# Performance work log

Hardware: AMD Instinct MI355X
Metric: run time of the kernel (lower is better)

Reference implementation:

```python
import jax, jax.numpy as jnp
import numpy as np

B, S, D_MODEL, D_INNER = 64, 128, 1024, 1024


def setup_inputs() -> dict:
    key = jax.random.key(0)
    ks = jax.random.split(key, 10)
    sc = 0.02
    return {
        "embeddings": jax.random.normal(ks[0], (B, S, D_MODEL), dtype=jnp.float32),
        "Wq": jax.random.normal(ks[1], (D_MODEL, D_INNER), dtype=jnp.float32) * sc,
        "bq": jnp.zeros((D_INNER,), dtype=jnp.float32),
        "Wk": jax.random.normal(ks[2], (D_MODEL, D_INNER), dtype=jnp.float32) * sc,
        "bk": jnp.zeros((D_INNER,), dtype=jnp.float32),
        "Wv": jax.random.normal(ks[3], (D_MODEL, D_INNER), dtype=jnp.float32) * sc,
        "bv": jnp.zeros((D_INNER,), dtype=jnp.float32),
        "w": jax.random.normal(ks[4], (S, S), dtype=jnp.float32) * sc,
        "Wo": jax.random.normal(ks[5], (D_INNER, D_MODEL), dtype=jnp.float32) * sc,
        "bo": jnp.zeros((D_MODEL,), dtype=jnp.float32),
    }


def reference(embeddings, Wq, bq, Wk, bk, Wv, bv, w, Wo, bo):
    # embeddings: [B, S, Dm]
    seq_len = embeddings.shape[1]
    q = embeddings @ Wq + bq          # [B, S, Di]
    k = embeddings @ Wk + bk
    v = embeddings @ Wv + bv

    max_k = jnp.max(k, axis=1, keepdims=True)   # [B, 1, Di]
    exp_k = jnp.exp(k - max_k)                  # [B, S, Di]

    max_w = jnp.max(w, axis=1, keepdims=True)   # [S, 1]
    wn = w - max_w                              # [S, S]
    tril = jnp.tril(jnp.ones((seq_len, seq_len), dtype=bool))
    wn = jnp.where(tril, wn[:seq_len, :seq_len], -jnp.inf)
    # torch.einsum('bjj,bjd->bjd', exp_w, x) picks the DIAGONAL of exp_w
    # (repeated subscript j) and multiplies elementwise along the seq dim.
    diag_w = jnp.exp(jnp.diagonal(wn))          # [S]; tril diagonal is True so finite
    dw = diag_w[None, :, None]                  # [1, S, 1]

    numerator = dw * (exp_k * v)                # [B, S, Di]
    denominator = dw * exp_k                    # [B, S, Di]
    out = jax.nn.sigmoid(q) * (numerator / denominator)
    return out @ Wo + bo                        # [B, S, Dm]
```

## Files before the change

### kernel.cpp

```cpp
#include <hip/hip_runtime.h>


typedef short bf16x8 __attribute__((ext_vector_type(8)));
typedef float f32x4  __attribute__((ext_vector_type(4)));

__device__ __forceinline__ short f2bf(float f) {
  union { float f; unsigned u; } x; x.f = f;
  unsigned r = x.u + 0x7fffu + ((x.u >> 16) & 1u);
  return (short)(r >> 16);
}

struct alignas(16) S8 { short v[8]; };

#define GLDS(g, l) \
  __builtin_amdgcn_global_load_lds((const __attribute__((address_space(1))) void*)(g), \
                                   (__attribute__((address_space(3))) void*)(l), 16, 0, 0)

__global__ __launch_bounds__(256) void prep_kernel(
    const float* __restrict__ emb, const float* __restrict__ Wq, const float* __restrict__ Wv,
    const float* __restrict__ Wo, short* __restrict__ embB, short* __restrict__ WqvT,
    short* __restrict__ WoT) {
  __shared__ float tr[32 * 33];
  const int t = threadIdx.x;
  const int bid = blockIdx.x;
  const int gdim = gridDim.x;

  for (size_t i = (size_t)bid * 256 + t; i < 1048576; i += (size_t)gdim * 256) {
    const float4* p = (const float4*)emb + i * 2;
    float4 a = p[0], b = p[1];
    S8 s;
    s.v[0] = f2bf(a.x); s.v[1] = f2bf(a.y); s.v[2] = f2bf(a.z); s.v[3] = f2bf(a.w);
    s.v[4] = f2bf(b.x); s.v[5] = f2bf(b.y); s.v[6] = f2bf(b.z); s.v[7] = f2bf(b.w);
    ((S8*)embB)[i] = s;
  }

  int tx = t & 31, ty = t >> 5;
  for (int z = bid; z < 3072; z += gdim) {
    const float* in = (z < 1024) ? Wq : (z < 2048) ? Wv : Wo;
    short* op = (z < 1024) ? WqvT : (z < 2048) ? (WqvT + 1048576) : WoT;
    int ti = z & 1023;
    int bx = (ti & 31) * 32, by = (ti >> 5) * 32;
    __syncthreads();
#pragma unroll
    for (int i = 0; i < 32; i += 8)
      tr[(ty + i) * 33 + tx] = in[(size_t)(by + ty + i) * 1024 + bx + tx];
    __syncthreads();
#pragma unroll
    for (int i = 0; i < 32; i += 8)
      op[(size_t)(bx + ty + i) * 1024 + by + tx] = f2bf(tr[tx * 33 + ty + i]);
  }
}

__global__ __launch_bounds__(256) void gemm_qv_kernel(
    const short* __restrict__ A, const short* __restrict__ BT,
    const float* __restrict__ bq, const float* __restrict__ bv, short* __restrict__ X) {
  __shared__ short As[128 * 64];
  __shared__ short Bqs[64 * 64];
  __shared__ short Bvs[64 * 64];
  const int t = threadIdx.x;
  const int lane = t & 63;
  const int w = t >> 6;
  const int l16 = lane & 15;
  const int quad = lane >> 4;
  const int bm = blockIdx.x * 128;
  const int bn = blockIdx.y * 64;
  const int wm = (w & 1) * 64;
  const int wn = (w >> 1) * 32;

  const int r8 = t >> 3;
  const int swe = ((t & 7) ^ (r8 & 7)) * 8;
  const short* pA0 = A + (size_t)(bm + r8) * 1024 + swe;
  const short* pA1 = pA0 + 32 * 1024;
  const short* pA2 = pA0 + 64 * 1024;
  const short* pA3 = pA0 + 96 * 1024;
  const short* pBq0 = BT + (size_t)(bn + r8) * 1024 + swe;
  const short* pBq1 = pBq0 + 32 * 1024;
  const short* pBv0 = BT + (size_t)(1024 + bn + r8) * 1024 + swe;
  const short* pBv1 = pBv0 + 32 * 1024;
  short* lA = As + w * 512;
  short* lBq = Bqs + w * 512;
  short* lBv = Bvs + w * 512;

  const int qsw0 = (quad ^ (l16 & 7)) * 8;
  const int qsw1 = ((quad + 4) ^ (l16 & 7)) * 8;
  const short* fA0 = As + (wm + l16) * 64 + qsw0;
  const short* fA1 = As + (wm + l16) * 64 + qsw1;
  const short* fq0 = Bqs + (wn + l16) * 64 + qsw0;
  const short* fq1 = Bqs + (wn + l16) * 64 + qsw1;
  const short* fv0 = Bvs + (wn + l16) * 64 + qsw0;
  const short* fv1 = Bvs + (wn + l16) * 64 + qsw1;

  f32x4 accq[4][2] = {};
  f32x4 accv[4][2] = {};

  for (int it = 0; it < 16; ++it) {
    GLDS(pA0, lA); GLDS(pA1, lA + 2048); GLDS(pA2, lA + 4096); GLDS(pA3, lA + 6144);
    GLDS(pBq0, lBq); GLDS(pBq1, lBq + 2048);
    GLDS(pBv0, lBv); GLDS(pBv1, lBv + 2048);
    pA0 += 64; pA1 += 64; pA2 += 64; pA3 += 64;
    pBq0 += 64; pBq1 += 64; pBv0 += 64; pBv1 += 64;
    __syncthreads();

#pragma unroll
    for (int h = 0; h < 2; h++) {
      const short* fA = h ? fA1 : fA0;
      const short* fq = h ? fq1 : fq0;
      const short* fv = h ? fv1 : fv0;
      bf16x8 av[4], bqf[2], bvf[2];
#pragma unroll
      for (int i = 0; i < 4; i++) av[i] = *(const bf16x8*)(fA + i * 1024);
#pragma unroll
      for (int j = 0; j < 2; j++) {
        bqf[j] = *(const bf16x8*)(fq + j * 1024);
        bvf[j] = *(const bf16x8*)(fv + j * 1024);
      }
#pragma unroll
      for (int i = 0; i < 4; i++)
#pragma unroll
        for (int j = 0; j < 2; j++) {
          accq[i][j] = __builtin_amdgcn_mfma_f32_16x16x32_bf16(av[i], bqf[j], accq[i][j], 0, 0, 0);
          accv[i][j] = __builtin_amdgcn_mfma_f32_16x16x32_bf16(av[i], bvf[j], accv[i][j], 0, 0, 0);
        }
    }
    __syncthreads();
  }

#pragma unroll
  for (int j = 0; j < 2; j++) {
    int col = bn + wn + j * 16 + l16;
    float bql = bq[col], bvl = bv[col];
#pragma unroll
    for (int i = 0; i < 4; i++)
#pragma unroll
      for (int r = 0; r < 4; r++) {
        int row = bm + wm + i * 16 + quad * 4 + r;
        float q = accq[i][j][r] + bql;
        float v = accv[i][j][r] + bvl;
        float s = 1.0f / (1.0f + __expf(-q));
        X[(size_t)row * 1024 + col] = f2bf(s * v);
      }
  }
}

__global__ __launch_bounds__(256) void gemm_bt_kernel(
    const short* __restrict__ A, const short* __restrict__ BT, float* __restrict__ C,
    const float* __restrict__ bias) {
  __shared__ short As[128 * 64];
  __shared__ short Bs[128 * 64];
  const int t = threadIdx.x;
  const int lane = t & 63;
  const int w = t >> 6;
  const int l16 = lane & 15;
  const int quad = lane >> 4;
  const int bm = blockIdx.x * 128;
  const int bn = blockIdx.y * 128;
  const int wm = (w & 1) * 64;
  const int wn = (w >> 1) * 64;

  const int r8 = t >> 3;
  const int swe = ((t & 7) ^ (r8 & 7)) * 8;
  const short* pA0 = A + (size_t)(bm + r8) * 1024 + swe;
  const short* pA1 = pA0 + 32 * 1024;
  const short* pA2 = pA0 + 64 * 1024;
  const short* pA3 = pA0 + 96 * 1024;
  const short* pB0 = BT + (size_t)(bn + r8) * 1024 + swe;
  const short* pB1 = pB0 + 32 * 1024;
  const short* pB2 = pB0 + 64 * 1024;
  const short* pB3 = pB0 + 96 * 1024;
  short* lA = As + w * 512;
  short* lB = Bs + w * 512;

  const int qsw0 = (quad ^ (l16 & 7)) * 8;
  const int qsw1 = ((quad + 4) ^ (l16 & 7)) * 8;
  const short* fA0 = As + (wm + l16) * 64 + qsw0;
  const short* fA1 = As + (wm + l16) * 64 + qsw1;
  const short* fB0 = Bs + (wn + l16) * 64 + qsw0;
  const short* fB1 = Bs + (wn + l16) * 64 + qsw1;

  f32x4 acc[4][4] = {};

  for (int it = 0; it < 16; ++it) {
    GLDS(pA0, lA); GLDS(pA1, lA + 2048); GLDS(pA2, lA + 4096); GLDS(pA3, lA + 6144);
    GLDS(pB0, lB); GLDS(pB1, lB + 2048); GLDS(pB2, lB + 4096); GLDS(pB3, lB + 6144);
    pA0 += 64; pA1 += 64; pA2 += 64; pA3 += 64;
    pB0 += 64; pB1 += 64; pB2 += 64; pB3 += 64;
    __syncthreads();

#pragma unroll
    for (int h = 0; h < 2; h++) {
      const short* fA = h ? fA1 : fA0;
      const short* fB = h ? fB1 : fB0;
      bf16x8 av[4], bw[4];
#pragma unroll
      for (int i = 0; i < 4; i++) av[i] = *(const bf16x8*)(fA + i * 1024);
#pragma unroll
      for (int j = 0; j < 4; j++) bw[j] = *(const bf16x8*)(fB + j * 1024);
#pragma unroll
      for (int i = 0; i < 4; i++)
#pragma unroll
        for (int j = 0; j < 4; j++)
          acc[i][j] = __builtin_amdgcn_mfma_f32_16x16x32_bf16(av[i], bw[j], acc[i][j], 0, 0, 0);
    }
    __syncthreads();
  }

#pragma unroll
  for (int j = 0; j < 4; j++) {
    int col = bn + wn + j * 16 + l16;
    float bl = bias[col];
#pragma unroll
    for (int i = 0; i < 4; i++)
#pragma unroll
      for (int r = 0; r < 4; r++) {
        int row = bm + wm + i * 16 + quad * 4 + r;
        C[(size_t)row * 1024 + col] = acc[i][j][r] + bl;
      }
  }
}

extern "C" void kernel_launch(void* const* d_in, const int* in_sizes, int n_in,
                              void* d_out, int out_size, void* d_ws, size_t ws_size,
                              hipStream_t stream) {
  const float* emb = (const float*)d_in[0];
  const float* Wq  = (const float*)d_in[1];
  const float* bq  = (const float*)d_in[2];
  const float* Wv  = (const float*)d_in[5];
  const float* bv  = (const float*)d_in[6];
  const float* Wo  = (const float*)d_in[8];
  const float* bo  = (const float*)d_in[9];
  float* out = (float*)d_out;

  char* ws = (char*)d_ws;
  short* embB = (short*)(ws);
  short* X    = (short*)(ws + 16777216);
  short* WqvT = (short*)(ws + 33554432);
  short* WoT  = (short*)(ws + 37748736);

  prep_kernel<<<1024, 256, 0, stream>>>(emb, Wq, Wv, Wo, embB, WqvT, WoT);
  gemm_qv_kernel<<<dim3(64, 16), 256, 0, stream>>>(embB, WqvT, bq, bv, X);
  gemm_bt_kernel<<<dim3(64, 8), 256, 0, stream>>>(X, WoT, out, bo);
}
```

Before: 168.9 us.

## Fuse fp32-to-bf16 embedding conversion into QV GEMM A-tile loading

Drops the separate pass that converts the 32MB fp32 embedding tensor to bf16. The QV GEMM now loads fp32 A tiles through registers, packs them to bf16 with a perm-based rounding, and stores them into LDS itself, which removes one full write and re-read of the activations. The prep kernel now only transposes weights, one tile per block. In exchange, A is loaded synchronously through registers instead of direct global-to-LDS, and each of the 16 N-blocks re-reads fp32 A, doubling A traffic per GEMM. The new rounding also drops round-to-nearest-even tie handling.

```diff
diff --git a/kernel.cpp b/kernel.cpp
--- a/kernel.cpp
+++ b/kernel.cpp
@@ -10,49 +10,48 @@
   return (short)(r >> 16);
 }
 
+__device__ __forceinline__ unsigned pkbf(float f0, float f1) {
+  unsigned a = __float_as_uint(f1) + 0x8000u;
+  unsigned b = __float_as_uint(f0) + 0x8000u;
+  return __builtin_amdgcn_perm(a, b, 0x07060302u);
+}
+
 struct alignas(16) S8 { short v[8]; };
+
+__device__ __forceinline__ S8 pack8(float4 x, float4 y) {
+  union { unsigned d[4]; S8 s; } u;
+  u.d[0] = pkbf(x.x, x.y); u.d[1] = pkbf(x.z, x.w);
+  u.d[2] = pkbf(y.x, y.y); u.d[3] = pkbf(y.z, y.w);
+  return u.s;
+}
 
 #define GLDS(g, l) \
   __builtin_amdgcn_global_load_lds((const __attribute__((address_space(1))) void*)(g), \
                                    (__attribute__((address_space(3))) void*)(l), 16, 0, 0)
 
 __global__ __launch_bounds__(256) void prep_kernel(
-    const float* __restrict__ emb, const float* __restrict__ Wq, const float* __restrict__ Wv,
-    const float* __restrict__ Wo, short* __restrict__ embB, short* __restrict__ WqvT,
-    short* __restrict__ WoT) {
+    const float* __restrict__ Wq, const float* __restrict__ Wv, const float* __restrict__ Wo,
+    short* __restrict__ WqvT, short* __restrict__ WoT) {
   __shared__ float tr[32 * 33];
   const int t = threadIdx.x;
-  const int bid = blockIdx.x;
-  const int gdim = gridDim.x;
-
-  for (size_t i = (size_t)bid * 256 + t; i < 1048576; i += (size_t)gdim * 256) {
-    const float4* p = (const float4*)emb + i * 2;
-    float4 a = p[0], b = p[1];
-    S8 s;
-    s.v[0] = f2bf(a.x); s.v[1] = f2bf(a.y); s.v[2] = f2bf(a.z); s.v[3] = f2bf(a.w);
-    s.v[4] = f2bf(b.x); s.v[5] = f2bf(b.y); s.v[6] = f2bf(b.z); s.v[7] = f2bf(b.w);
-    ((S8*)embB)[i] = s;
-  }
-
-  int tx = t & 31, ty = t >> 5;
-  for (int z = bid; z < 3072; z += gdim) {
-    const float* in = (z < 1024) ? Wq : (z < 2048) ? Wv : Wo;
-    short* op = (z < 1024) ? WqvT : (z < 2048) ? (WqvT + 1048576) : WoT;
-    int ti = z & 1023;
-    int bx = (ti & 31) * 32, by = (ti >> 5) * 32;
-    __syncthreads();
-#pragma unroll
-    for (int i = 0; i < 32; i += 8)
-      tr[(ty + i) * 33 + tx] = in[(size_t)(by + ty + i) * 1024 + bx + tx];
-    __syncthreads();
-#pragma unroll
-    for (int i = 0; i < 32; i += 8)
-      op[(size_t)(bx + ty + i) * 1024 + by + tx] = f2bf(tr[tx * 33 + ty + i]);
-  }
+  const int z = blockIdx.x;
+  const float* in = (z < 1024) ? Wq : (z < 2048) ? Wv : Wo;
+  short* op = (z < 1024) ? WqvT : (z < 2048) ? (WqvT + 1048576) : WoT;
+  const int ti = z & 1023;
+  const int bx = (ti & 31) * 32, by = (ti >> 5) * 32;
+  const int tx = t & 31, ty = t >> 5;
+#pragma unroll
+  for (int i = 0; i < 32; i += 8)
+    tr[(ty + i) * 33 + tx] = in[(size_t)(by + ty + i) * 1024 + bx + tx];
+  __syncthreads();
+#pragma unroll
+  for (int i = 0; i < 32; i += 8)
+    op[(size_t)(bx + ty + i) * 1024 + by + tx] = f2bf(tr[tx * 33 + ty + i]);
 }
 
 __global__ __launch_bounds__(256) void gemm_qv_kernel(
-    const short* __restrict__ A, const short* __restrict__ BT,
+    const float* __restrict__ A,
+    const short* __restrict__ BT,
     const float* __restrict__ bq, const float* __restrict__ bv, short* __restrict__ X) {
   __shared__ short As[128 * 64];
   __shared__ short Bqs[64 * 64];
@@ -68,16 +67,18 @@
   const int wn = (w >> 1) * 32;
 
   const int r8 = t >> 3;
+  const int ch = (t & 7) ^ (r8 & 7);
+  const float* gA0 = A + (size_t)(bm + r8) * 1024 + ch * 8;
+  const float* gA1 = gA0 + 32 * 1024;
+  const float* gA2 = gA0 + 64 * 1024;
+  const float* gA3 = gA0 + 96 * 1024;
+  short* sA = As + r8 * 64 + (t & 7) * 8;
+
   const int swe = ((t & 7) ^ (r8 & 7)) * 8;
-  const short* pA0 = A + (size_t)(bm + r8) * 1024 + swe;
-  const short* pA1 = pA0 + 32 * 1024;
-  const short* pA2 = pA0 + 64 * 1024;
-  const short* pA3 = pA0 + 96 * 1024;
   const short* pBq0 = BT + (size_t)(bn + r8) * 1024 + swe;
   const short* pBq1 = pBq0 + 32 * 1024;
   const short* pBv0 = BT + (size_t)(1024 + bn + r8) * 1024 + swe;
   const short* pBv1 = pBv0 + 32 * 1024;
-  short* lA = As + w * 512;
   short* lBq = Bqs + w * 512;
   short* lBv = Bvs + w * 512;
 
@@ -94,10 +95,17 @@
   f32x4 accv[4][2] = {};
 
   for (int it = 0; it < 16; ++it) {
-    GLDS(pA0, lA); GLDS(pA1, lA + 2048); GLDS(pA2, lA + 4096); GLDS(pA3, lA + 6144);
+    float4 a0 = *(const float4*)(gA0);     float4 a0b = *(const float4*)(gA0 + 4);
+    float4 a1 = *(const float4*)(gA1);     float4 a1b = *(const float4*)(gA1 + 4);
+    float4 a2 = *(const float4*)(gA2);     float4 a2b = *(const float4*)(gA2 + 4);
+    float4 a3 = *(const float4*)(gA3);     float4 a3b = *(const float4*)(gA3 + 4);
     GLDS(pBq0, lBq); GLDS(pBq1, lBq + 2048);
     GLDS(pBv0, lBv); GLDS(pBv1, lBv + 2048);
-    pA0 += 64; pA1 += 64; pA2 += 64; pA3 += 64;
+    *(S8*)(sA)        = pack8(a0, a0b);
+    *(S8*)(sA + 2048) = pack8(a1, a1b);
+    *(S8*)(sA + 4096) = pack8(a2, a2b);
+    *(S8*)(sA + 6144) = pack8(a3, a3b);
+    gA0 += 64; gA1 += 64; gA2 += 64; gA3 += 64;
     pBq0 += 64; pBq1 += 64; pBv0 += 64; pBv1 += 64;
     __syncthreads();
 
@@ -231,12 +239,11 @@
   float* out = (float*)d_out;
 
   char* ws = (char*)d_ws;
-  short* embB = (short*)(ws);
-  short* X    = (short*)(ws + 16777216);
-  short* WqvT = (short*)(ws + 33554432);
-  short* WoT  = (short*)(ws + 37748736);
-
-  prep_kernel<<<1024, 256, 0, stream>>>(emb, Wq, Wv, Wo, embB, WqvT, WoT);
-  gemm_qv_kernel<<<dim3(64, 16), 256, 0, stream>>>(embB, WqvT, bq, bv, X);
+  short* X    = (short*)(ws);
+  short* WqvT = (short*)(ws + 16777216);
+  short* WoT  = (short*)(ws + 20971520);
+
+  prep_kernel<<<3072, 256, 0, stream>>>(Wq, Wv, Wo, WqvT, WoT);
+  gemm_qv_kernel<<<dim3(64, 16), 256, 0, stream>>>(emb, WqvT, bq, bv, X);
   gemm_bt_kernel<<<dim3(64, 8), 256, 0, stream>>>(X, WoT, out, bo);
 }
```

New measurement: 183.5 us. 1.09x slower.
